# Performance work log

Hardware: AMD Instinct MI355X
Metric: run time of the kernel (lower is better)

The kernel has to match this reference:

```python
import jax, jax.numpy as jnp
import numpy as np

KE = 14.3996
ALPHA = 0.3
CUTOFF = 10.0
K_MAX = 6
N_ATOMS = 100000
N_PAIRS = 6400000
N_MOL = 64


def _generate_kvecs():
    kr = np.arange(0, K_MAX + 1, dtype=np.float32)
    kr = np.concatenate([kr, -kr[1:]])
    # cartesian product of (kr, kr, kr)
    g = np.stack(np.meshgrid(kr, kr, kr, indexing='ij'), axis=-1).reshape(-1, 3)
    norm = (g ** 2).sum(axis=1)
    mask = (norm <= K_MAX ** 2 + 2) & (norm != 0)
    return jnp.asarray(g[mask])  # [1020, 3]


def setup_inputs() -> dict:
    key = jax.random.key(0)
    k1, k2, k3, k4, k5, k6, k7 = jax.random.split(key, 7)
    partial_charges = jax.random.normal(k1, (N_ATOMS, 1), dtype=jnp.float32)
    # pair displacement vectors; scale so typical |r_ij| ~ 3-6 A, avoids d ~ 0
    Rij = jax.random.normal(k2, (N_PAIRS, 3), dtype=jnp.float32) * 3.0 + 1.0
    R = jax.random.uniform(k3, (N_ATOMS, 3), dtype=jnp.float32) * 20.0
    # orthorhombic-ish invertible cells: diag(~20) + small perturbation
    cell = jnp.eye(3, dtype=jnp.float32)[None] * 20.0 \
        + jax.random.uniform(k4, (N_MOL, 3, 3), dtype=jnp.float32) * 0.1
    idx_m = jnp.sort(jax.random.randint(k5, (N_ATOMS,), 0, N_MOL)).astype(jnp.int64)
    idx_i = jax.random.randint(k6, (N_PAIRS,), 0, N_ATOMS).astype(jnp.int64)
    idx_j = jax.random.randint(k7, (N_PAIRS,), 0, N_ATOMS).astype(jnp.int64)
    kvecs = _generate_kvecs()
    return {"partial_charges": partial_charges, "Rij": Rij, "R": R, "cell": cell,
            "kvecs": kvecs, "idx_m": idx_m, "idx_i": idx_i, "idx_j": idx_j}


def reference(partial_charges, Rij, R, cell, kvecs, idx_m, idx_i, idx_j):
    q = partial_charges.squeeze(-1)                      # [A]
    d_ij = jnp.linalg.norm(Rij, axis=1)                  # [P]
    sqrt_a = jnp.sqrt(jnp.float32(ALPHA))

    # ---- real space: gather q, erfc-screened pair potential, double scatter ----
    f_r = jax.scipy.special.erfc(sqrt_a * d_ij) / d_ij
    f_r_cut = jax.scipy.special.erfc(sqrt_a * CUTOFF) / CUTOFF
    pot_ij = q[idx_i] * q[idx_j] * (f_r - f_r_cut)
    pot_ij = jnp.where(d_ij <= CUTOFF, pot_ij, jnp.zeros_like(pot_ij))
    y_atom = jax.ops.segment_sum(pot_ij, idx_i, num_segments=N_ATOMS)
    y_real = 0.5 * KE * jax.ops.segment_sum(y_atom, idx_m, num_segments=N_MOL)

    # ---- reciprocal space ----
    two_pi = 2.0 * jnp.float32(np.pi)
    recip_box = two_pi * jnp.transpose(jnp.linalg.inv(cell), (0, 2, 1))  # [M,3,3]
    v_box = jnp.abs(jnp.linalg.det(cell))                                # [M]
    prefactor = two_pi / v_box
    kv = jnp.einsum('kd,mde->mke', kvecs, recip_box)     # [M,K,3]
    k_sq = jnp.sum(kv ** 2, axis=2)                      # [M,K]
    q_gauss = jnp.exp(-0.25 * k_sq / ALPHA)              # [M,K]
    # per-atom phase: gather per-molecule k-vectors, dot with positions
    kdp = jnp.einsum('akd,ad->ak', kv[idx_m], R)         # [A,K]
    q_real = jax.ops.segment_sum(q[:, None] * jnp.cos(kdp), idx_m, num_segments=N_MOL)
    q_imag = jax.ops.segment_sum(q[:, None] * jnp.sin(kdp), idx_m, num_segments=N_MOL)
    q_dens = q_real ** 2 + q_imag ** 2                   # [M,K]
    y_ewald = prefactor * jnp.sum(q_dens * q_gauss / k_sq, axis=1)
    self_int = jnp.sqrt(ALPHA / np.pi) * jax.ops.segment_sum(q ** 2, idx_m, num_segments=N_MOL)
    y_recip = KE * (y_ewald - self_int)

    return y_real + y_recip                              # [M]
```

## Files before the change

kernel.cpp:

```cpp
#include <hip/hip_runtime.h>
#include <math.h>

#define KE_C     14.3996f
#define ALPHA_C  0.3f
#define CUTOFF_C 10.0f
#define TWO_PI_C 6.283185307179586f
#define RBLOCKS  2048
#define KSPL     4
#define ASPL     4

__global__ __launch_bounds__(64) void k_cell(const float* __restrict__ cell,
                                             float* __restrict__ RB,
                                             float* __restrict__ VB, int nmol) {
    int m = blockIdx.x * blockDim.x + threadIdx.x;
    if (m >= nmol) return;
    const float* c = cell + m * 9;
    float a00 = c[0], a01 = c[1], a02 = c[2];
    float a10 = c[3], a11 = c[4], a12 = c[5];
    float a20 = c[6], a21 = c[7], a22 = c[8];
    float det = a00 * (a11 * a22 - a12 * a21)
              - a01 * (a10 * a22 - a12 * a20)
              + a02 * (a10 * a21 - a11 * a20);
    float id = 1.0f / det;
    float inv00 = (a11 * a22 - a12 * a21) * id;
    float inv01 = (a02 * a21 - a01 * a22) * id;
    float inv02 = (a01 * a12 - a02 * a11) * id;
    float inv10 = (a12 * a20 - a10 * a22) * id;
    float inv11 = (a00 * a22 - a02 * a20) * id;
    float inv12 = (a02 * a10 - a00 * a12) * id;
    float inv20 = (a10 * a21 - a11 * a20) * id;
    float inv21 = (a01 * a20 - a00 * a21) * id;
    float inv22 = (a00 * a11 - a01 * a10) * id;
    float* rb = RB + m * 9;
    rb[0] = TWO_PI_C * inv00; rb[1] = TWO_PI_C * inv10; rb[2] = TWO_PI_C * inv20;
    rb[3] = TWO_PI_C * inv01; rb[4] = TWO_PI_C * inv11; rb[5] = TWO_PI_C * inv21;
    rb[6] = TWO_PI_C * inv02; rb[7] = TWO_PI_C * inv12; rb[8] = TWO_PI_C * inv22;
    VB[m] = fabsf(det);
}

__global__ __launch_bounds__(128) void k_bounds(const int* __restrict__ idx_m,
                                                int* __restrict__ bounds,
                                                int natoms, int nmol) {
    int m = threadIdx.x;
    if (m > nmol) return;
    int lo = 0, hi = natoms;
    while (lo < hi) {
        int mid = (lo + hi) >> 1;
        if (idx_m[mid] < m) lo = mid + 1; else hi = mid;
    }
    bounds[m] = lo;
}

__global__ __launch_bounds__(256) void k_atoms(const float* __restrict__ R,
                                               const float* __restrict__ q,
                                               const int* __restrict__ idx_m,
                                               const float* __restrict__ RB,
                                               float4* __restrict__ S4,
                                               float2* __restrict__ QM,
                                               float* __restrict__ SI, int natoms) {
    __shared__ float si[64];
    int tid = threadIdx.x;
    if (tid < 64) si[tid] = 0.0f;
    __syncthreads();
    int a = blockIdx.x * 256 + tid;
    if (a < natoms) {
        int m = idx_m[a];
        float r0 = R[3 * a], r1 = R[3 * a + 1], r2 = R[3 * a + 2];
        const float* rb = RB + m * 9;
        float s0 = rb[0] * r0 + rb[1] * r1 + rb[2] * r2;
        float s1 = rb[3] * r0 + rb[4] * r1 + rb[5] * r2;
        float s2 = rb[6] * r0 + rb[7] * r1 + rb[8] * r2;
        float qa = q[a];
        S4[a] = make_float4(s0, s1, s2, qa);
        QM[a] = make_float2(qa, __int_as_float(m));
        atomicAdd(&si[m & 63], qa * qa);
    }
    __syncthreads();
    if (tid < 64) atomicAdd(&SI[tid], si[tid]);
}

__global__ __launch_bounds__(256) void k_real(const float* __restrict__ Rij,
                                              const int* __restrict__ idx_i,
                                              const int* __restrict__ idx_j,
                                              const float2* __restrict__ QM,
                                              float* __restrict__ YRpad, int npairs) {
    __shared__ float acc[4][64];
    int tid = threadIdx.x;
    int wave = tid >> 6;
    if (tid < 256) { acc[tid >> 6][tid & 63] = 0.0f; }
    __syncthreads();
    const float sqa = 0.5477225575051661f;
    const float frcut = erfcf(sqa * CUTOFF_C) / CUTOFF_C;
    int nchunk = npairs >> 2;
    int stride = gridDim.x * 256;
    for (int c = blockIdx.x * 256 + tid; c < nchunk; c += stride) {
        int p = c << 2;
        int4 ii = *(const int4*)(idx_i + p);
        int4 jj = *(const int4*)(idx_j + p);
        const float4* r4 = (const float4*)(Rij + 3 * p);
        float4 ra = r4[0], rb = r4[1], rc = r4[2];
        float x0 = ra.x, y0 = ra.y, z0 = ra.z;
        float x1 = ra.w, y1 = rb.x, z1 = rb.y;
        float x2 = rb.z, y2 = rb.w, z2 = rc.x;
        float x3 = rc.y, y3 = rc.z, z3 = rc.w;
        float2 qi0 = QM[ii.x], qi1 = QM[ii.y], qi2 = QM[ii.z], qi3 = QM[ii.w];
        float2 qj0 = QM[jj.x], qj1 = QM[jj.y], qj2 = QM[jj.z], qj3 = QM[jj.w];
        float d0 = sqrtf(x0 * x0 + y0 * y0 + z0 * z0);
        float d1 = sqrtf(x1 * x1 + y1 * y1 + z1 * z1);
        float d2 = sqrtf(x2 * x2 + y2 * y2 + z2 * z2);
        float d3 = sqrtf(x3 * x3 + y3 * y3 + z3 * z3);
        if (d0 <= CUTOFF_C)
            atomicAdd(&acc[wave][__float_as_int(qi0.y) & 63],
                      qi0.x * qj0.x * (erfcf(sqa * d0) / d0 - frcut));
        if (d1 <= CUTOFF_C)
            atomicAdd(&acc[wave][__float_as_int(qi1.y) & 63],
                      qi1.x * qj1.x * (erfcf(sqa * d1) / d1 - frcut));
        if (d2 <= CUTOFF_C)
            atomicAdd(&acc[wave][__float_as_int(qi2.y) & 63],
                      qi2.x * qj2.x * (erfcf(sqa * d2) / d2 - frcut));
        if (d3 <= CUTOFF_C)
            atomicAdd(&acc[wave][__float_as_int(qi3.y) & 63],
                      qi3.x * qj3.x * (erfcf(sqa * d3) / d3 - frcut));
    }
    if (blockIdx.x == 0 && tid == 0) {
        for (int p = nchunk << 2; p < npairs; ++p) {
            float x = Rij[3 * p], y = Rij[3 * p + 1], z = Rij[3 * p + 2];
            float d = sqrtf(x * x + y * y + z * z);
            if (d <= CUTOFF_C) {
                float2 qi = QM[idx_i[p]];
                float2 qj = QM[idx_j[p]];
                atomicAdd(&acc[0][__float_as_int(qi.y) & 63],
                          qi.x * qj.x * (erfcf(sqa * d) / d - frcut));
            }
        }
    }
    __syncthreads();
    if (tid < 64) {
        float v = acc[0][tid] + acc[1][tid] + acc[2][tid] + acc[3][tid];
        atomicAdd(&YRpad[tid * 16], v);
    }
}

__global__ __launch_bounds__(256) void k_recip(const float4* __restrict__ S4,
                                               const float* __restrict__ kvecs,
                                               const int* __restrict__ bounds,
                                               float* __restrict__ QR,
                                               float* __restrict__ QI, int nk) {
    __shared__ float4 tile[256];
    int tid = threadIdx.x;
    int b = blockIdx.x;
    int m  = b / (KSPL * ASPL);
    int rem = b % (KSPL * ASPL);
    int kc = rem / ASPL;
    int ac = rem % ASPL;
    int s0 = bounds[m], s1 = bounds[m + 1];
    int na = s1 - s0;
    int per = (na + ASPL - 1) / ASPL;
    int a0 = s0 + ac * per;
    int a1 = min(a0 + per, s1);
    int k = kc * 256 + tid;
    float kx = 0.f, ky = 0.f, kz = 0.f;
    if (k < nk) { kx = kvecs[3 * k]; ky = kvecs[3 * k + 1]; kz = kvecs[3 * k + 2]; }
    float qr = 0.f, qi = 0.f;
    for (int t0 = a0; t0 < a1; t0 += 256) {
        __syncthreads();
        int a = t0 + tid;
        if (a < a1) tile[tid] = S4[a];
        __syncthreads();
        int n = min(256, a1 - t0);
#pragma unroll 4
        for (int t = 0; t < n; ++t) {
            float4 s = tile[t];
            float ph = kx * s.x + ky * s.y + kz * s.z;
            float sn, cs;
            __sincosf(ph, &sn, &cs);
            qr += s.w * cs;
            qi += s.w * sn;
        }
    }
    if (k < nk) {
        atomicAdd(&QR[m * nk + k], qr);
        atomicAdd(&QI[m * nk + k], qi);
    }
}

__global__ __launch_bounds__(256) void k_final(const float* __restrict__ kvecs,
                                               const float* __restrict__ RB,
                                               const float* __restrict__ VB,
                                               const float* __restrict__ QR,
                                               const float* __restrict__ QI,
                                               const float* __restrict__ YRpad,
                                               const float* __restrict__ SI,
                                               float* __restrict__ out, int nk) {
    int m = blockIdx.x;
    int tid = threadIdx.x;
    __shared__ float rb[9];
    __shared__ float wsum[4];
    if (tid < 9) rb[tid] = RB[m * 9 + tid];
    __syncthreads();
    float acc = 0.0f;
    for (int k = tid; k < nk; k += 256) {
        float gx = kvecs[3 * k], gy = kvecs[3 * k + 1], gz = kvecs[3 * k + 2];
        float kv0 = gx * rb[0] + gy * rb[3] + gz * rb[6];
        float kv1 = gx * rb[1] + gy * rb[4] + gz * rb[7];
        float kv2 = gx * rb[2] + gy * rb[5] + gz * rb[8];
        float ksq = kv0 * kv0 + kv1 * kv1 + kv2 * kv2;
        float qr = QR[m * nk + k], qi = QI[m * nk + k];
        acc += (qr * qr + qi * qi) * __expf(-0.25f / ALPHA_C * ksq) / ksq;
    }
#pragma unroll
    for (int off = 32; off > 0; off >>= 1) acc += __shfl_down(acc, off, 64);
    if ((tid & 63) == 0) wsum[tid >> 6] = acc;
    __syncthreads();
    if (tid == 0) {
        float s = wsum[0] + wsum[1] + wsum[2] + wsum[3];
        float pref = TWO_PI_C / VB[m];
        float self_c = sqrtf(ALPHA_C / 3.14159265358979323846f);
        out[m] = 0.5f * KE_C * YRpad[m * 16] + KE_C * (pref * s - self_c * SI[m]);
    }
}

extern "C" void kernel_launch(void* const* d_in, const int* in_sizes, int n_in,
                              void* d_out, int out_size, void* d_ws, size_t ws_size,
                              hipStream_t stream) {
    const float* q     = (const float*)d_in[0];
    const float* Rij   = (const float*)d_in[1];
    const float* R     = (const float*)d_in[2];
    const float* cell  = (const float*)d_in[3];
    const float* kvecs = (const float*)d_in[4];
    const int*   idx_m = (const int*)d_in[5];
    const int*   idx_i = (const int*)d_in[6];
    const int*   idx_j = (const int*)d_in[7];

    int natoms = in_sizes[0];
    int npairs = in_sizes[1] / 3;
    int nmol   = in_sizes[3] / 9;
    int nk     = in_sizes[4] / 3;
    float* out = (float*)d_out;

    float* W      = (float*)d_ws;
    float* RB     = W;
    float* VB     = RB + 576;
    int*   bounds = (int*)(VB + 64);
    float4* S4    = (float4*)(W + 720);
    float2* QM    = (float2*)(W + 720 + 4 * (size_t)natoms);
    float* QR     = W + 720 + 6 * (size_t)natoms;
    float* QI     = QR + (size_t)nmol * nk;
    float* SI     = QI + (size_t)nmol * nk;
    float* YRpad  = SI + 64;

    size_t zero_bytes = ((size_t)2 * nmol * nk + 64 + 64 * 16) * sizeof(float);
    hipMemsetAsync(QR, 0, zero_bytes, stream);

    k_cell  <<<1, 64, 0, stream>>>(cell, RB, VB, nmol);
    k_bounds<<<1, 128, 0, stream>>>(idx_m, bounds, natoms, nmol);
    k_atoms <<<(natoms + 255) / 256, 256, 0, stream>>>(R, q, idx_m, RB, S4, QM, SI, natoms);
    k_real  <<<RBLOCKS, 256, 0, stream>>>(Rij, idx_i, idx_j, QM, YRpad, npairs);
    k_recip <<<nmol * KSPL * ASPL, 256, 0, stream>>>(S4, kvecs, bounds, QR, QI, nk);
    k_final <<<nmol, 256, 0, stream>>>(kvecs, RB, VB, QR, QI, YRpad, SI, out, nk);
}
```

Measured before the change: 272.6 us.

## Fuse real-space and reciprocal kernels into one launch with fast erfc

```diff
diff --git a/kernel.cpp b/kernel.cpp
--- a/kernel.cpp
+++ b/kernel.cpp
@@ -5,9 +5,21 @@
 #define ALPHA_C  0.3f
 #define CUTOFF_C 10.0f
 #define TWO_PI_C 6.283185307179586f
-#define RBLOCKS  2048
 #define KSPL     4
 #define ASPL     4
+#define NRECIP   1024
+
+typedef float vfloat4 __attribute__((ext_vector_type(4)));
+typedef int   vint4   __attribute__((ext_vector_type(4)));
+
+__device__ __forceinline__ float fast_erfc(float x) {
+    float t = __builtin_amdgcn_rcpf(fmaf(0.3275911f, x, 1.0f));
+    float p = fmaf(t, 1.061405429f, -1.453152027f);
+    p = fmaf(t, p, 1.421413741f);
+    p = fmaf(t, p, -0.284496736f);
+    p = fmaf(t, p, 0.254829592f);
+    return t * p * __expf(-x * x);
+}
 
 __global__ __launch_bounds__(64) void k_cell(const float* __restrict__ cell,
                                              float* __restrict__ RB,
@@ -79,108 +91,107 @@
     if (tid < 64) atomicAdd(&SI[tid], si[tid]);
 }
 
-__global__ __launch_bounds__(256) void k_real(const float* __restrict__ Rij,
+__global__ __launch_bounds__(256) void k_main(const float4* __restrict__ S4,
+                                              const float* __restrict__ kvecs,
+                                              const int* __restrict__ bounds,
+                                              float* __restrict__ QR,
+                                              float* __restrict__ QI, int nk,
+                                              const float* __restrict__ Rij,
                                               const int* __restrict__ idx_i,
                                               const int* __restrict__ idx_j,
                                               const float2* __restrict__ QM,
                                               float* __restrict__ YRpad, int npairs) {
     __shared__ float acc[4][64];
     int tid = threadIdx.x;
-    int wave = tid >> 6;
-    if (tid < 256) { acc[tid >> 6][tid & 63] = 0.0f; }
-    __syncthreads();
-    const float sqa = 0.5477225575051661f;
-    const float frcut = erfcf(sqa * CUTOFF_C) / CUTOFF_C;
-    int nchunk = npairs >> 2;
-    int stride = gridDim.x * 256;
-    for (int c = blockIdx.x * 256 + tid; c < nchunk; c += stride) {
-        int p = c << 2;
-        int4 ii = *(const int4*)(idx_i + p);
-        int4 jj = *(const int4*)(idx_j + p);
-        const float4* r4 = (const float4*)(Rij + 3 * p);
-        float4 ra = r4[0], rb = r4[1], rc = r4[2];
-        float x0 = ra.x, y0 = ra.y, z0 = ra.z;
-        float x1 = ra.w, y1 = rb.x, z1 = rb.y;
-        float x2 = rb.z, y2 = rb.w, z2 = rc.x;
-        float x3 = rc.y, y3 = rc.z, z3 = rc.w;
-        float2 qi0 = QM[ii.x], qi1 = QM[ii.y], qi2 = QM[ii.z], qi3 = QM[ii.w];
-        float2 qj0 = QM[jj.x], qj1 = QM[jj.y], qj2 = QM[jj.z], qj3 = QM[jj.w];
-        float d0 = sqrtf(x0 * x0 + y0 * y0 + z0 * z0);
-        float d1 = sqrtf(x1 * x1 + y1 * y1 + z1 * z1);
-        float d2 = sqrtf(x2 * x2 + y2 * y2 + z2 * z2);
-        float d3 = sqrtf(x3 * x3 + y3 * y3 + z3 * z3);
-        if (d0 <= CUTOFF_C)
-            atomicAdd(&acc[wave][__float_as_int(qi0.y) & 63],
-                      qi0.x * qj0.x * (erfcf(sqa * d0) / d0 - frcut));
-        if (d1 <= CUTOFF_C)
-            atomicAdd(&acc[wave][__float_as_int(qi1.y) & 63],
-                      qi1.x * qj1.x * (erfcf(sqa * d1) / d1 - frcut));
-        if (d2 <= CUTOFF_C)
-            atomicAdd(&acc[wave][__float_as_int(qi2.y) & 63],
-                      qi2.x * qj2.x * (erfcf(sqa * d2) / d2 - frcut));
-        if (d3 <= CUTOFF_C)
-            atomicAdd(&acc[wave][__float_as_int(qi3.y) & 63],
-                      qi3.x * qj3.x * (erfcf(sqa * d3) / d3 - frcut));
-    }
-    if (blockIdx.x == 0 && tid == 0) {
-        for (int p = nchunk << 2; p < npairs; ++p) {
-            float x = Rij[3 * p], y = Rij[3 * p + 1], z = Rij[3 * p + 2];
-            float d = sqrtf(x * x + y * y + z * z);
-            if (d <= CUTOFF_C) {
-                float2 qi = QM[idx_i[p]];
-                float2 qj = QM[idx_j[p]];
-                atomicAdd(&acc[0][__float_as_int(qi.y) & 63],
-                          qi.x * qj.x * (erfcf(sqa * d) / d - frcut));
-            }
-        }
-    }
-    __syncthreads();
-    if (tid < 64) {
-        float v = acc[0][tid] + acc[1][tid] + acc[2][tid] + acc[3][tid];
-        atomicAdd(&YRpad[tid * 16], v);
-    }
-}
-
-__global__ __launch_bounds__(256) void k_recip(const float4* __restrict__ S4,
-                                               const float* __restrict__ kvecs,
-                                               const int* __restrict__ bounds,
-                                               float* __restrict__ QR,
-                                               float* __restrict__ QI, int nk) {
-    __shared__ float4 tile[256];
-    int tid = threadIdx.x;
-    int b = blockIdx.x;
-    int m  = b / (KSPL * ASPL);
-    int rem = b % (KSPL * ASPL);
-    int kc = rem / ASPL;
-    int ac = rem % ASPL;
-    int s0 = bounds[m], s1 = bounds[m + 1];
-    int na = s1 - s0;
-    int per = (na + ASPL - 1) / ASPL;
-    int a0 = s0 + ac * per;
-    int a1 = min(a0 + per, s1);
-    int k = kc * 256 + tid;
-    float kx = 0.f, ky = 0.f, kz = 0.f;
-    if (k < nk) { kx = kvecs[3 * k]; ky = kvecs[3 * k + 1]; kz = kvecs[3 * k + 2]; }
-    float qr = 0.f, qi = 0.f;
-    for (int t0 = a0; t0 < a1; t0 += 256) {
-        __syncthreads();
-        int a = t0 + tid;
-        if (a < a1) tile[tid] = S4[a];
-        __syncthreads();
-        int n = min(256, a1 - t0);
+    int bid = blockIdx.x;
+
+    if (bid < NRECIP) {
+        int m  = bid >> 4;
+        int kc = (bid >> 2) & 3;
+        int ac = bid & 3;
+        int s0 = bounds[m], s1 = bounds[m + 1];
+        int per = (s1 - s0 + ASPL - 1) / ASPL;
+        int a0 = s0 + ac * per;
+        int a1 = min(a0 + per, s1);
+        int k = kc * 256 + tid;
+        float kx = 0.f, ky = 0.f, kz = 0.f;
+        if (k < nk) { kx = kvecs[3 * k]; ky = kvecs[3 * k + 1]; kz = kvecs[3 * k + 2]; }
+        float qr = 0.f, qi = 0.f;
 #pragma unroll 4
-        for (int t = 0; t < n; ++t) {
-            float4 s = tile[t];
-            float ph = kx * s.x + ky * s.y + kz * s.z;
+        for (int t = a0; t < a1; ++t) {
+            float4 s = S4[t];
+            float ph = fmaf(kx, s.x, fmaf(ky, s.y, kz * s.z));
             float sn, cs;
             __sincosf(ph, &sn, &cs);
-            qr += s.w * cs;
-            qi += s.w * sn;
-        }
-    }
-    if (k < nk) {
-        atomicAdd(&QR[m * nk + k], qr);
-        atomicAdd(&QI[m * nk + k], qi);
+            qr = fmaf(s.w, cs, qr);
+            qi = fmaf(s.w, sn, qi);
+        }
+        if (k < nk) {
+            atomicAdd(&QR[m * nk + k], qr);
+            atomicAdd(&QI[m * nk + k], qi);
+        }
+    } else {
+        int wave = tid >> 6;
+        ((float*)acc)[tid] = 0.0f;
+        __syncthreads();
+        const float sqa = 0.5477225575051661f;
+        const float frcut = fast_erfc(sqa * CUTOFF_C) / CUTOFF_C;
+        long base = ((long)(bid - NRECIP) * 256 + tid) << 3;
+        if (base + 8 <= npairs) {
+            vint4 ii0 = __builtin_nontemporal_load((const vint4*)(idx_i + base));
+            vint4 ii1 = __builtin_nontemporal_load((const vint4*)(idx_i + base) + 1);
+            vint4 jj0 = __builtin_nontemporal_load((const vint4*)(idx_j + base));
+            vint4 jj1 = __builtin_nontemporal_load((const vint4*)(idx_j + base) + 1);
+            const vfloat4* r4 = (const vfloat4*)(Rij + 3 * base);
+            vfloat4 A = __builtin_nontemporal_load(r4 + 0);
+            vfloat4 B = __builtin_nontemporal_load(r4 + 1);
+            vfloat4 C = __builtin_nontemporal_load(r4 + 2);
+            vfloat4 D = __builtin_nontemporal_load(r4 + 3);
+            vfloat4 E = __builtin_nontemporal_load(r4 + 4);
+            vfloat4 F = __builtin_nontemporal_load(r4 + 5);
+            float2 qa0 = QM[ii0.x], qa1 = QM[ii0.y], qa2 = QM[ii0.z], qa3 = QM[ii0.w];
+            float2 qa4 = QM[ii1.x], qa5 = QM[ii1.y], qa6 = QM[ii1.z], qa7 = QM[ii1.w];
+            float2 qb0 = QM[jj0.x], qb1 = QM[jj0.y], qb2 = QM[jj0.z], qb3 = QM[jj0.w];
+            float2 qb4 = QM[jj1.x], qb5 = QM[jj1.y], qb6 = QM[jj1.z], qb7 = QM[jj1.w];
+#define PAIR(xx, yy, zz, qa, qb)                                              \
+            {                                                                 \
+                float d2 = fmaf(xx, xx, fmaf(yy, yy, (zz) * (zz)));           \
+                if (d2 <= CUTOFF_C * CUTOFF_C) {                              \
+                    float rd = __builtin_amdgcn_rsqf(d2);                     \
+                    float d = d2 * rd;                                        \
+                    float f = fast_erfc(sqa * d) * rd - frcut;                \
+                    atomicAdd(&acc[wave][__float_as_int((qa).y) & 63],        \
+                              (qa).x * (qb).x * f);                           \
+                }                                                             \
+            }
+            PAIR(A.x, A.y, A.z, qa0, qb0)
+            PAIR(A.w, B.x, B.y, qa1, qb1)
+            PAIR(B.z, B.w, C.x, qa2, qb2)
+            PAIR(C.y, C.z, C.w, qa3, qb3)
+            PAIR(D.x, D.y, D.z, qa4, qb4)
+            PAIR(D.w, E.x, E.y, qa5, qb5)
+            PAIR(E.z, E.w, F.x, qa6, qb6)
+            PAIR(F.y, F.z, F.w, qa7, qb7)
+#undef PAIR
+        } else if (base < npairs) {
+            for (long p = base; p < npairs; ++p) {
+                float x = Rij[3 * p], y = Rij[3 * p + 1], z = Rij[3 * p + 2];
+                float d2 = fmaf(x, x, fmaf(y, y, z * z));
+                if (d2 <= CUTOFF_C * CUTOFF_C) {
+                    float rd = __builtin_amdgcn_rsqf(d2);
+                    float d = d2 * rd;
+                    float2 qi2 = QM[idx_i[p]];
+                    float2 qj2 = QM[idx_j[p]];
+                    atomicAdd(&acc[wave][__float_as_int(qi2.y) & 63],
+                              qi2.x * qj2.x * (fast_erfc(sqa * d) * rd - frcut));
+                }
+            }
+        }
+        __syncthreads();
+        if (tid < 64) {
+            float v = acc[0][tid] + acc[1][tid] + acc[2][tid] + acc[3][tid];
+            atomicAdd(&YRpad[tid * 16], v);
+        }
     }
 }
 
@@ -250,12 +261,13 @@
     float* YRpad  = SI + 64;
 
     size_t zero_bytes = ((size_t)2 * nmol * nk + 64 + 64 * 16) * sizeof(float);
-    hipMemsetAsync(QR, 0, zero_bytes, stream);
-
+    (void)hipMemsetAsync(QR, 0, zero_bytes, stream);
+
+    int nrb = (npairs + 2047) / 2048;
     k_cell  <<<1, 64, 0, stream>>>(cell, RB, VB, nmol);
     k_bounds<<<1, 128, 0, stream>>>(idx_m, bounds, natoms, nmol);
     k_atoms <<<(natoms + 255) / 256, 256, 0, stream>>>(R, q, idx_m, RB, S4, QM, SI, natoms);
-    k_real  <<<RBLOCKS, 256, 0, stream>>>(Rij, idx_i, idx_j, QM, YRpad, npairs);
-    k_recip <<<nmol * KSPL * ASPL, 256, 0, stream>>>(S4, kvecs, bounds, QR, QI, nk);
+    k_main  <<<NRECIP + nrb, 256, 0, stream>>>(S4, kvecs, bounds, QR, QI, nk,
+                                               Rij, idx_i, idx_j, QM, YRpad, npairs);
     k_final <<<nmol, 256, 0, stream>>>(kvecs, RB, VB, QR, QI, YRpad, SI, out, nk);
 }
```

After: 264.7 us. 1.03x faster.
